# Performance work log

Hardware: AMD Instinct MI355X
Metric: run time of the kernel (lower is better)

## Reference

```python
import jax, jax.numpy as jnp
import numpy as np
import math

EMBED_DIMS = 256
NUM_LANDMARKS = 40  # hard-coded k=40 in the original module
B, N = 2, 8192


def setup_inputs() -> dict:
    key = jax.random.key(0)
    ks = jax.random.split(key, 9)
    C = EMBED_DIMS
    w = lambda k: jax.random.normal(k, (C, C), dtype=jnp.float32) * 0.02
    b = lambda k: jax.random.normal(k, (C,), dtype=jnp.float32) * 0.02
    return {
        "query": jax.random.normal(ks[0], (B, N, C), dtype=jnp.float32),
        "Wq": w(ks[1]), "bq": b(ks[2]),
        "Wk": w(ks[3]), "bk": b(ks[4]),
        "Wv": w(ks[5]), "bv": b(ks[6]),
        "Wo": w(ks[7]), "bo": b(ks[8]),
    }


def reference(query, Wq, bq, Wk, bk, Wv, bv, Wo, bo):
    # key = value = identity = query (defaults in the original forward)
    C = query.shape[-1]
    scaling = math.sqrt(C)

    q = query @ Wq.T + bq  # [B, N, C]
    k = query @ Wk.T + bk
    v = query @ Wv.T + bv

    # Full similarity only to score keys: score_m[b, m] = sum_n sim_nm[b, n, m]
    sim_nm = jnp.einsum('bnc,bmc->bnm', q, k) / scaling  # [B, N, N]
    score_m = sim_nm.sum(axis=1)                          # [B, N]

    _, top_idx = jax.lax.top_k(score_m, NUM_LANDMARKS)    # [B, 40]
    selected = jnp.take_along_axis(k, top_idx[:, :, None], axis=1)  # [B, 40, C]

    sim_qn = jax.nn.softmax(jnp.einsum('bnc,bkc->bnk', q, selected) / scaling, axis=-1)  # [B, N, 40]
    sim_km = jax.nn.softmax(jnp.einsum('bmc,bkc->bmk', k, selected) / scaling, axis=-1)  # [B, N, 40]

    sim_qk = jnp.einsum('bnk,bmk->bnm', sim_qn, sim_km)   # [B, N, N]
    out = jnp.einsum('bnm,bmc->bnc', sim_qk, v)           # [B, N, C]
    out = out @ Wo.T + bo
    return query + out  # identity residual; dropouts are identity at p=0
```

## Files before the change

kernel.cpp:

```cpp
#include <hip/hip_runtime.h>
#include <cstddef>
#include <cstdint>

#define BATCH 2
#define SEQ 8192
#define CH 256
#define NLM 40
#define NLMP 48
#define MROWS (BATCH * SEQ)
#define INV_SCALE 0.0625f
#define NCBLK 256

typedef unsigned short ushort_t;
typedef __attribute__((ext_vector_type(8))) short short8;
typedef __attribute__((ext_vector_type(4))) float floatx4;

__device__ __forceinline__ ushort_t f2bf(float f) {
    unsigned int u = __float_as_uint(f);
    u += 0x7FFFu + ((u >> 16) & 1u);
    return (ushort_t)(u >> 16);
}
__device__ __forceinline__ float bf2f(ushort_t u) {
    return __uint_as_float(((unsigned)u) << 16);
}

__global__ __launch_bounds__(256) void convert_colsum(const float* __restrict__ x,
                                                      ushort_t* __restrict__ xbf,
                                                      float* __restrict__ partial) {
    __shared__ float red[4][256];
    const int b = blockIdx.y;
    const int r0 = blockIdx.x * 32;
    const int t = threadIdx.x;
    const int c4 = (t & 63) * 4;
    const int rg = t >> 6;
    const float* base = x + ((size_t)b * SEQ + r0) * 256;
    ushort_t* obase = xbf + ((size_t)b * SEQ + r0) * 256;
    float4 s = {0.f, 0.f, 0.f, 0.f};
#pragma unroll
    for (int i = 0; i < 8; i++) {
        const int r = rg + i * 4;
        const float4 a = *(const float4*)&base[(size_t)r * 256 + c4];
        uint2 o;
        o.x = f2bf(a.x) | ((unsigned)f2bf(a.y) << 16);
        o.y = f2bf(a.z) | ((unsigned)f2bf(a.w) << 16);
        *(uint2*)&obase[(size_t)r * 256 + c4] = o;
        s.x += a.x; s.y += a.y; s.z += a.z; s.w += a.w;
    }
    *(float4*)&red[rg][c4] = s;
    __syncthreads();
    const float tot = red[0][t] + red[1][t] + red[2][t] + red[3][t];
    partial[((size_t)b * NCBLK + blockIdx.x) * 256 + t] = tot;
}

__global__ __launch_bounds__(1024) void ws_kernel(const float* __restrict__ partial,
                                                  const float* __restrict__ Wq,
                                                  const float* __restrict__ bq,
                                                  const float* __restrict__ Wk,
                                                  float* __restrict__ ws,
                                                  float* __restrict__ tmat) {
    const int b = blockIdx.x;
    __shared__ float xs[256];
    __shared__ float qs[256];
    __shared__ float ppart[4][256];
    const int t = threadIdx.x;
    {
        float* tz = tmat + (size_t)b * NLM * 256;
        for (int i = t; i < NLM * 256; i += 1024) tz[i] = 0.f;
    }
    {
        const int c = t & 255, qd = t >> 8;
        const float* pb = partial + ((size_t)b * NCBLK + qd * 64) * 256 + c;
        float a = 0.f;
#pragma unroll 8
        for (int i = 0; i < 64; i++) a += pb[(size_t)i * 256];
        ppart[qd][c] = a;
    }
    __syncthreads();
    if (t < 256) xs[t] = ppart[0][t] + ppart[1][t] + ppart[2][t] + ppart[3][t];
    __syncthreads();
    const int lane = t & 63, w = t >> 6;
    for (int g = 0; g < 16; g++) {
        const int o = w * 16 + g;
        const float4 wq = *(const float4*)&Wq[(size_t)o * 256 + lane * 4];
        const float4 x4 = *(const float4*)&xs[lane * 4];
        float d = wq.x * x4.x + wq.y * x4.y + wq.z * x4.z + wq.w * x4.w;
#pragma unroll
        for (int off = 32; off >= 1; off >>= 1) d += __shfl_down(d, off);
        if (lane == 0) qs[o] = d + 8192.0f * bq[o];
    }
    __syncthreads();
    const int c = t & 255, part = t >> 8;
    float a = 0.f;
    for (int o = part * 64; o < part * 64 + 64; o++)
        a += Wk[(size_t)o * 256 + c] * qs[o];
    ppart[part][c] = a;
    __syncthreads();
    if (t < 256)
        ws[b * 256 + t] = ppart[0][t] + ppart[1][t] + ppart[2][t] + ppart[3][t];
}

__global__ __launch_bounds__(256) void gemm_qkv_score(const ushort_t* __restrict__ xbf,
                                                      const float* __restrict__ Wq,
                                                      const float* __restrict__ Wk,
                                                      const float* __restrict__ Wv,
                                                      const float* __restrict__ bq,
                                                      const float* __restrict__ bk,
                                                      const float* __restrict__ bv,
                                                      ushort_t* __restrict__ qkv,
                                                      const float* __restrict__ query,
                                                      const float* __restrict__ ws,
                                                      float* __restrict__ score) {
    __shared__ __align__(16) ushort_t As[128 * 72];
    __shared__ __align__(16) ushort_t Bs[64 * 40];
    const int z = blockIdx.z;
    const int t = threadIdx.x;
    const int lane = t & 63;
    const int w = t >> 6;

    if (z == 3) {
        const int blk = blockIdx.y * 4 + blockIdx.x;
#pragma unroll
        for (int i = 0; i < 8; i++) {
            const int g = blk * 32 + i * 4 + w;
            const int b = g >> 13;
            const int m = g & 8191;
            const float4 kv = *(const float4*)&query[(size_t)g * 256 + lane * 4];
            const float4 qs = *(const float4*)&ws[b * 256 + lane * 4];
            float d = kv.x * qs.x + kv.y * qs.y + kv.z * qs.z + kv.w * qs.w;
#pragma unroll
            for (int off = 32; off >= 1; off >>= 1) d += __shfl_down(d, off);
            if (lane == 0) score[(size_t)b * SEQ + m] = d * INV_SCALE;
        }
        return;
    }

    const float* __restrict__ W = (z == 0) ? Wq : (z == 1) ? Wk : Wv;
    const float* __restrict__ bias = (z == 0) ? bq : (z == 1) ? bk : bv;
    ushort_t* __restrict__ out = qkv + (size_t)z * MROWS * 256;
    const int o0 = blockIdx.x * 64;
    const int m0 = blockIdx.y * 128;
    const int quad = lane >> 4;
    const int l16 = lane & 15;

    floatx4 acc[2][4];
#pragma unroll
    for (int rt = 0; rt < 2; rt++)
#pragma unroll
        for (int ct = 0; ct < 4; ct++) acc[rt][ct] = (floatx4){0.f, 0.f, 0.f, 0.f};

    for (int kc = 0; kc < 256; kc += 32) {
#pragma unroll
        for (int u = 0; u < 2; u++) {
            const int cid = t + u * 256;
            const int row = cid >> 2, off = cid & 3;
            *(uint4*)&As[row * 40 + off * 8] =
                *(const uint4*)&xbf[(size_t)(m0 + row) * 256 + kc + off * 8];
        }
        {
            const int row = t >> 2, off = t & 3;
            const float* wp = &W[(size_t)(o0 + row) * 256 + kc + off * 8];
            const float4 a = *(const float4*)wp;
            const float4 c = *(const float4*)(wp + 4);
            uint4 o;
            o.x = f2bf(a.x) | ((unsigned)f2bf(a.y) << 16);
            o.y = f2bf(a.z) | ((unsigned)f2bf(a.w) << 16);
            o.z = f2bf(c.x) | ((unsigned)f2bf(c.y) << 16);
            o.w = f2bf(c.z) | ((unsigned)f2bf(c.w) << 16);
            *(uint4*)&Bs[row * 40 + off * 8] = o;
        }
        __syncthreads();
        short8 a[2], b[4];
#pragma unroll
        for (int rt = 0; rt < 2; rt++)
            a[rt] = *(const short8*)&As[(w * 32 + rt * 16 + l16) * 40 + quad * 8];
#pragma unroll
        for (int ct = 0; ct < 4; ct++)
            b[ct] = *(const short8*)&Bs[(ct * 16 + l16) * 40 + quad * 8];
#pragma unroll
        for (int rt = 0; rt < 2; rt++)
#pragma unroll
            for (int ct = 0; ct < 4; ct++)
                acc[rt][ct] = __builtin_amdgcn_mfma_f32_16x16x32_bf16(
                    a[rt], b[ct], acc[rt][ct], 0, 0, 0);
        __syncthreads();
    }

#pragma unroll
    for (int rt = 0; rt < 2; rt++) {
#pragma unroll
        for (int ct = 0; ct < 4; ct++) {
            const int col = ct * 16 + l16;
            const float bb = bias[o0 + col];
#pragma unroll
            for (int reg = 0; reg < 4; reg++) {
                const int row = w * 32 + rt * 16 + quad * 4 + reg;
                As[row * 72 + col] = f2bf(acc[rt][ct][reg] + bb);
            }
        }
    }
    __syncthreads();
#pragma unroll
    for (int u = 0; u < 4; u++) {
        const int cid = t + u * 256;
        const int row = cid >> 3;
        const int off = (cid & 7) * 8;
        *(uint4*)&out[(size_t)(m0 + row) * 256 + o0 + off] =
            *(const uint4*)&As[row * 72 + off];
    }
}

__global__ __launch_bounds__(1024) void topk_gather(const float* __restrict__ score,
                                                    const ushort_t* __restrict__ kmat,
                                                    ushort_t* __restrict__ sel) {
    const int b = blockIdx.x;
    const int t = threadIdx.x;
    __shared__ unsigned hist[256];
    __shared__ unsigned wsum[64];
    __shared__ unsigned sPrefix, sMask, sRem, sNeq;
    __shared__ int sNgt;
    __shared__ int top[NLM];
    __shared__ unsigned topkey[NLM];

    unsigned key[8];
#pragma unroll
    for (int j = 0; j < 8; j++) {
        const unsigned u = __float_as_uint(score[(size_t)b * SEQ + t + j * 1024]);
        key[j] = u ^ (unsigned)(((int)u >> 31) | 0x80000000);
    }
    if (t == 0) { sPrefix = 0; sMask = 0; sRem = NLM; sNgt = 0; sNeq = 0; }

    for (int lvl = 0; lvl < 4; lvl++) {
        const int shift = 24 - 8 * lvl;
        if (t < 256) hist[t] = 0;
        __syncthreads();
        const unsigned pfx = sPrefix, msk = sMask;
#pragma unroll
        for (int j = 0; j < 8; j++)
            if (((key[j] ^ pfx) & msk) == 0)
                atomicAdd(&hist[(key[j] >> shift) & 255u], 1u);
        __syncthreads();
        if (t < 64) wsum[t] = hist[t * 4] + hist[t * 4 + 1] + hist[t * 4 + 2] + hist[t * 4 + 3];
        __syncthreads();
        if (t == 0) {
            unsigned rem = sRem, cum = 0;
            int g = 63;
            for (; g > 0; g--) { if (cum + wsum[g] >= rem) break; cum += wsum[g]; }
            int d = g * 4 + 3;
            for (; d > g * 4; d--) { if (cum + hist[d] >= rem) break; cum += hist[d]; }
            sRem = rem - cum;
            sPrefix |= ((unsigned)d) << shift;
            sMask |= 255u << shift;
        }
        __syncthreads();
    }
    const unsigned K40 = sPrefix;
    const unsigned rem = sRem;
    const int ngt = NLM - (int)rem;

#pragma unroll
    for (int j = 0; j < 8; j++) {
        if (key[j] > K40) {
            const int slot = atomicAdd(&sNgt, 1);
            top[slot] = t + j * 1024; topkey[slot] = key[j];
        } else if (key[j] == K40) {
            const unsigned e = atomicAdd(&sNeq, 1u);
            if (e < rem) {
                const int slot = ngt + (int)e;
                top[slot] = t + j * 1024; topkey[slot] = key[j];
            }
        }
    }
    __syncthreads();

    if (t < 64) {
        unsigned long long c = (t < NLM)
            ? ((((unsigned long long)(~topkey[t])) << 32) | (unsigned)top[t])
            : 0xFFFFFFFFFFFFFFFFull;
#pragma unroll
        for (int kk = 2; kk <= 64; kk <<= 1) {
#pragma unroll
            for (int j = kk >> 1; j >= 1; j >>= 1) {
                const unsigned long long o = __shfl_xor(c, j);
                const bool takeMin = ((t & kk) == 0) == ((t & j) == 0);
                const bool less = c < o;
                c = (takeMin == less) ? c : o;
            }
        }
        if (t < NLM) top[t] = (int)(c & 0xFFFFFFFFu);
    }
    __syncthreads();

    for (int f = t; f < NLMP * 256; f += 1024) {
        const int j = f >> 8;
        const int cc = f & 255;
        sel[(size_t)b * NLMP * 256 + f] =
            (j < NLM) ? kmat[((size_t)b * SEQ + top[j]) * 256 + cc] : (ushort_t)0;
    }
}

__global__ __launch_bounds__(256, 4) void sim_fused(const ushort_t* __restrict__ qbf,
                                                    const ushort_t* __restrict__ kbf,
                                                    const ushort_t* __restrict__ vbf,
                                                    const ushort_t* __restrict__ sel,
                                                    float* __restrict__ simq,
                                                    float* __restrict__ tmat) {
    __shared__ __align__(16) char smem[43008];
    float (*Ps)[40]  = (float(*)[40])smem;
    ushort_t* Vs     = (ushort_t*)(smem + 10240);
    const int b = blockIdx.y;
    const int n0 = blockIdx.x * 64;
    const int t = threadIdx.x;
    const int lane = t & 63;
    const int w = t >> 6;
    const int quad = lane >> 4;
    const int l16 = lane & 15;
    const ushort_t* __restrict__ A = (blockIdx.z == 0) ? qbf : kbf;
    const ushort_t* __restrict__ Arow = A + ((size_t)b * SEQ + n0 + w * 16 + l16) * 256;
    const ushort_t* __restrict__ Sb = sel + (size_t)b * NLMP * 256 + (size_t)l16 * 256;

    floatx4 acc[3];
#pragma unroll
    for (int ct = 0; ct < 3; ct++) acc[ct] = (floatx4){0.f, 0.f, 0.f, 0.f};

#pragma unroll
    for (int ks = 0; ks < 8; ks++) {
        const int ko = ks * 32 + quad * 8;
        const short8 a  = *(const short8*)&Arow[ko];
        const short8 b0 = *(const short8*)&Sb[ko];
        const short8 b1 = *(const short8*)&Sb[16 * 256 + ko];
        const short8 b2 = *(const short8*)&Sb[32 * 256 + ko];
        acc[0] = __builtin_amdgcn_mfma_f32_16x16x32_bf16(a, b0, acc[0], 0, 0, 0);
        acc[1] = __builtin_amdgcn_mfma_f32_16x16x32_bf16(a, b1, acc[1], 0, 0, 0);
        acc[2] = __builtin_amdgcn_mfma_f32_16x16x32_bf16(a, b2, acc[2], 0, 0, 0);
    }

    const bool v2ok = (l16 < 8);
    float p0[4], p1[4], p2[4];
#pragma unroll
    for (int reg = 0; reg < 4; reg++) {
        const float l0 = acc[0][reg] * INV_SCALE;
        const float l1 = acc[1][reg] * INV_SCALE;
        const float l2 = acc[2][reg] * INV_SCALE;
        float m = fmaxf(l0, l1);
        if (v2ok) m = fmaxf(m, l2);
        m = fmaxf(m, __shfl_xor(m, 1));
        m = fmaxf(m, __shfl_xor(m, 2));
        m = fmaxf(m, __shfl_xor(m, 4));
        m = fmaxf(m, __shfl_xor(m, 8));
        const float e0 = expf(l0 - m);
        const float e1 = expf(l1 - m);
        const float e2 = v2ok ? expf(l2 - m) : 0.f;
        float s = e0 + e1 + e2;
        s += __shfl_xor(s, 1);
        s += __shfl_xor(s, 2);
        s += __shfl_xor(s, 4);
        s += __shfl_xor(s, 8);
        const float inv = 1.f / s;
        p0[reg] = e0 * inv; p1[reg] = e1 * inv; p2[reg] = e2 * inv;
    }

    const int row0 = w * 16 + quad * 4;
    if (blockIdx.z == 0) {
        float* __restrict__ dst = &simq[((size_t)b * SEQ + n0 + row0) * NLM];
#pragma unroll
        for (int reg = 0; reg < 4; reg++) {
            float* __restrict__ d2 = dst + reg * NLM;
            d2[l16] = p0[reg];
            d2[16 + l16] = p1[reg];
            if (v2ok) d2[32 + l16] = p2[reg];
        }
        return;
    }

#pragma unroll
    for (int reg = 0; reg < 4; reg++) {
        Ps[row0 + reg][l16] = p0[reg];
        Ps[row0 + reg][16 + l16] = p1[reg];
        if (v2ok) Ps[row0 + reg][32 + l16] = p2[reg];
    }
#pragma unroll
    for (int u = 0; u < 8; u++) {
        const int cid = t + u * 256;
        const int row = cid >> 5, off = (cid & 31) * 8;
        *(uint4*)&Vs[row * 256 + off] =
            *(const uint4*)&vbf[((size_t)b * SEQ + n0 + row) * 256 + off];
    }
    __syncthreads();

    float tac[40];
#pragma unroll
    for (int j = 0; j < 40; j++) tac[j] = 0.f;

#pragma unroll 2
    for (int m = 0; m < 64; m++) {
        const float vv = bf2f(Vs[m * 256 + t]);
#pragma unroll
        for (int j4 = 0; j4 < 10; j4++) {
            const float4 p = *(const float4*)&Ps[m][j4 * 4];
            tac[j4 * 4 + 0] = fmaf(p.x, vv, tac[j4 * 4 + 0]);
            tac[j4 * 4 + 1] = fmaf(p.y, vv, tac[j4 * 4 + 1]);
            tac[j4 * 4 + 2] = fmaf(p.z, vv, tac[j4 * 4 + 2]);
            tac[j4 * 4 + 3] = fmaf(p.w, vv, tac[j4 * 4 + 3]);
        }
    }
#pragma unroll
    for (int j = 0; j < 40; j++)
        atomicAdd(&tmat[(size_t)b * NLM * 256 + j * 256 + t], tac[j]);
}

__global__ __launch_bounds__(256) void out_pre_kernel(const float* __restrict__ simq,
                                                      const float* __restrict__ tmat,
                                                      ushort_t* __restrict__ outp_bf) {
    __shared__ float Pm[64][40];
    const int g0 = blockIdx.x * 64;
    const int b = g0 >> 13;
    const int t = threadIdx.x;
    float* pflat = &Pm[0][0];
    for (int f = t; f < 64 * NLM; f += 256) pflat[f] = simq[(size_t)g0 * NLM + f];
    float tc[40];
#pragma unroll
    for (int l = 0; l < 40; l++) tc[l] = tmat[(size_t)b * NLM * 256 + l * 256 + t];
    __syncthreads();
#pragma unroll 2
    for (int m = 0; m < 64; m++) {
        float a = 0.f;
#pragma unroll
        for (int j4 = 0; j4 < 10; j4++) {
            const float4 p = *(const float4*)&Pm[m][j4 * 4];
            a = fmaf(p.x, tc[j4 * 4 + 0], a);
            a = fmaf(p.y, tc[j4 * 4 + 1], a);
            a = fmaf(p.z, tc[j4 * 4 + 2], a);
            a = fmaf(p.w, tc[j4 * 4 + 3], a);
        }
        outp_bf[((size_t)g0 + m) * 256 + t] = f2bf(a);
    }
}

__global__ __launch_bounds__(256) void gemm_out(const ushort_t* __restrict__ Abf,
                                                const float* __restrict__ Wo,
                                                const float* __restrict__ bias,
                                                const float* __restrict__ resid,
                                                float* __restrict__ out) {
    __shared__ __align__(16) char smem[128 * 68 * 4];
    ushort_t* As = (ushort_t*)smem;
    ushort_t* Bs = (ushort_t*)(smem + 128 * 40 * 2);
    float* Ft = (float*)smem;
    const int t = threadIdx.x;
    const int o0 = blockIdx.x * 64;
    const int m0 = blockIdx.y * 128;
    const int lane = t & 63;
    const int w = t >> 6;
    const int quad = lane >> 4;
    const int l16 = lane & 15;

    floatx4 acc[2][4];
#pragma unroll
    for (int rt = 0; rt < 2; rt++)
#pragma unroll
        for (int ct = 0; ct < 4; ct++) acc[rt][ct] = (floatx4){0.f, 0.f, 0.f, 0.f};

    for (int kc = 0; kc < 256; kc += 32) {
#pragma unroll
        for (int u = 0; u < 2; u++) {
            const int cid = t + u * 256;
            const int row = cid >> 2, off = cid & 3;
            *(uint4*)&As[row * 40 + off * 8] =
                *(const uint4*)&Abf[(size_t)(m0 + row) * 256 + kc + off * 8];
        }
        {
            const int row = t >> 2, off = t & 3;
            const float* wp = &Wo[(size_t)(o0 + row) * 256 + kc + off * 8];
            const float4 a = *(const float4*)wp;
            const float4 c = *(const float4*)(wp + 4);
            uint4 o;
            o.x = f2bf(a.x) | ((unsigned)f2bf(a.y) << 16);
            o.y = f2bf(a.z) | ((unsigned)f2bf(a.w) << 16);
            o.z = f2bf(c.x) | ((unsigned)f2bf(c.y) << 16);
            o.w = f2bf(c.z) | ((unsigned)f2bf(c.w) << 16);
            *(uint4*)&Bs[row * 40 + off * 8] = o;
        }
        __syncthreads();
        short8 a[2], b[4];
#pragma unroll
        for (int rt = 0; rt < 2; rt++)
            a[rt] = *(const short8*)&As[(w * 32 + rt * 16 + l16) * 40 + quad * 8];
#pragma unroll
        for (int ct = 0; ct < 4; ct++)
            b[ct] = *(const short8*)&Bs[(ct * 16 + l16) * 40 + quad * 8];
#pragma unroll
        for (int rt = 0; rt < 2; rt++)
#pragma unroll
            for (int ct = 0; ct < 4; ct++)
                acc[rt][ct] = __builtin_amdgcn_mfma_f32_16x16x32_bf16(
                    a[rt], b[ct], acc[rt][ct], 0, 0, 0);
        __syncthreads();
    }

#pragma unroll
    for (int rt = 0; rt < 2; rt++) {
#pragma unroll
        for (int ct = 0; ct < 4; ct++) {
            const int col = ct * 16 + l16;
            const float bb = bias[o0 + col];
#pragma unroll
            for (int reg = 0; reg < 4; reg++) {
                const int row = w * 32 + rt * 16 + quad * 4 + reg;
                Ft[row * 68 + col] = acc[rt][ct][reg] + bb;
            }
        }
    }
    __syncthreads();
#pragma unroll
    for (int u = 0; u < 8; u++) {
        const int cid = t + u * 256;
        const int row = cid >> 4;
        const int off = (cid & 15) * 4;
        const float4 v = *(const float4*)&Ft[row * 68 + off];
        const float4 r4 = *(const float4*)&resid[(size_t)(m0 + row) * 256 + o0 + off];
        float4 o;
        o.x = v.x + r4.x; o.y = v.y + r4.y; o.z = v.z + r4.z; o.w = v.w + r4.w;
        *(float4*)&out[(size_t)(m0 + row) * 256 + o0 + off] = o;
    }
}

extern "C" void kernel_launch(void* const* d_in, const int* in_sizes, int n_in,
                              void* d_out, int out_size, void* d_ws, size_t ws_size,
                              hipStream_t stream) {
    const float* query = (const float*)d_in[0];
    const float* Wq = (const float*)d_in[1];
    const float* bq = (const float*)d_in[2];
    const float* Wk = (const float*)d_in[3];
    const float* bk = (const float*)d_in[4];
    const float* Wv = (const float*)d_in[5];
    const float* bv = (const float*)d_in[6];
    const float* Wo = (const float*)d_in[7];
    const float* bo = (const float*)d_in[8];
    float* out = (float*)d_out;

    char* p = (char*)d_ws;
    float* simq  = (float*)p;            p += (size_t)MROWS * NLM * 4;
    ushort_t* selbf = (ushort_t*)p;      p += (size_t)BATCH * NLMP * 256 * 2;
    float* tmat  = (float*)p;            p += (size_t)BATCH * NLM * 256 * 4;
    float* partial = (float*)p;          p += (size_t)BATCH * NCBLK * 256 * 4;
    float* ws    = (float*)p;            p += (size_t)BATCH * 256 * 4;
    float* score = (float*)p;            p += (size_t)BATCH * SEQ * 4;
    ushort_t* qkv = (ushort_t*)p;        p += (size_t)3 * MROWS * 256 * 2;
    ushort_t* xbf = (ushort_t*)p;        p += (size_t)MROWS * 256 * 2;
    ushort_t* qbf = qkv;
    ushort_t* kbf = qkv + (size_t)MROWS * 256;
    ushort_t* vbf = qkv + (size_t)2 * MROWS * 256;
    ushort_t* outp_bf = xbf;

    const dim3 blk(256);

    convert_colsum<<<dim3(SEQ / 32, BATCH), blk, 0, stream>>>(query, xbf, partial);
    ws_kernel<<<dim3(BATCH), dim3(1024), 0, stream>>>(partial, Wq, bq, Wk, ws, tmat);

    gemm_qkv_score<<<dim3(4, MROWS / 128, 4), blk, 0, stream>>>(
        xbf, Wq, Wk, Wv, bq, bk, bv, qkv, query, ws, score);

    topk_gather<<<dim3(BATCH), dim3(1024), 0, stream>>>(score, kbf, selbf);

    sim_fused<<<dim3(SEQ / 64, BATCH, 2), blk, 0, stream>>>(qbf, kbf, vbf, selbf, simq, tmat);

    out_pre_kernel<<<dim3(MROWS / 64), blk, 0, stream>>>(simq, tmat, outp_bf);
    gemm_out<<<dim3(4, MROWS / 128), blk, 0, stream>>>(outp_bf, Wo, bo, query, out);
}
```

Before: 196.7 us.

## Use direct global-to-LDS loads with XOR-swizzled tiles and deeper K step in GEMMs

The QKV and output-projection GEMMs now load the bf16 activation tiles straight into LDS with global_load_lds instead of staging them through registers. The LDS tiles widen to K=64 with an XOR swizzle in place of padding, which halves the number of barrier-separated iterations and aims to avoid bank conflicts. The V tile load in the attention kernel also switches to direct-to-LDS loads. The trade-offs are more LDS per block and a dependence on the swizzle indexing matching the wave-uniform LDS base addressing of the async load.

```diff
diff --git a/kernel.cpp b/kernel.cpp
--- a/kernel.cpp
+++ b/kernel.cpp
@@ -22,6 +22,12 @@
 }
 __device__ __forceinline__ float bf2f(ushort_t u) {
     return __uint_as_float(((unsigned)u) << 16);
+}
+
+__device__ __forceinline__ void gload_lds16(const ushort_t* g, ushort_t* l) {
+    __builtin_amdgcn_global_load_lds(
+        (const __attribute__((address_space(1))) unsigned int*)g,
+        (__attribute__((address_space(3))) unsigned int*)l, 16, 0, 0);
 }
 
 __global__ __launch_bounds__(256) void convert_colsum(const float* __restrict__ x,
@@ -110,8 +116,10 @@
                                                       const float* __restrict__ query,
                                                       const float* __restrict__ ws,
                                                       float* __restrict__ score) {
-    __shared__ __align__(16) ushort_t As[128 * 72];
-    __shared__ __align__(16) ushort_t Bs[64 * 40];
+    __shared__ __align__(16) char smem[24576];
+    ushort_t* As = (ushort_t*)smem;
+    ushort_t* Bs = (ushort_t*)(smem + 16384);
+    ushort_t* Es = (ushort_t*)smem;
     const int z = blockIdx.z;
     const int t = threadIdx.x;
     const int lane = t & 63;
@@ -141,6 +149,7 @@
     const int m0 = blockIdx.y * 128;
     const int quad = lane >> 4;
     const int l16 = lane & 15;
+    const int xsw = l16 & 7;
 
     floatx4 acc[2][4];
 #pragma unroll
@@ -148,17 +157,20 @@
 #pragma unroll
         for (int ct = 0; ct < 4; ct++) acc[rt][ct] = (floatx4){0.f, 0.f, 0.f, 0.f};
 
-    for (int kc = 0; kc < 256; kc += 32) {
+    for (int kc = 0; kc < 256; kc += 64) {
+#pragma unroll
+        for (int q = 0; q < 4; q++) {
+            const int r0 = w * 32 + q * 8;
+            gload_lds16(&xbf[(size_t)(m0 + r0 + (lane >> 3)) * 256 + kc +
+                             (((lane & 7) ^ (lane >> 3)) * 8)],
+                        &As[r0 * 64]);
+        }
 #pragma unroll
         for (int u = 0; u < 2; u++) {
             const int cid = t + u * 256;
-            const int row = cid >> 2, off = cid & 3;
-            *(uint4*)&As[row * 40 + off * 8] =
-                *(const uint4*)&xbf[(size_t)(m0 + row) * 256 + kc + off * 8];
-        }
-        {
-            const int row = t >> 2, off = t & 3;
-            const float* wp = &W[(size_t)(o0 + row) * 256 + kc + off * 8];
+            const int row = cid >> 3;
+            const int cch = cid & 7;
+            const float* wp = &W[(size_t)(o0 + row) * 256 + kc + cch * 8];
             const float4 a = *(const float4*)wp;
             const float4 c = *(const float4*)(wp + 4);
             uint4 o;
@@ -166,22 +178,27 @@
             o.y = f2bf(a.z) | ((unsigned)f2bf(a.w) << 16);
             o.z = f2bf(c.x) | ((unsigned)f2bf(c.y) << 16);
             o.w = f2bf(c.z) | ((unsigned)f2bf(c.w) << 16);
-            *(uint4*)&Bs[row * 40 + off * 8] = o;
-        }
-        __syncthreads();
-        short8 a[2], b[4];
-#pragma unroll
-        for (int rt = 0; rt < 2; rt++)
-            a[rt] = *(const short8*)&As[(w * 32 + rt * 16 + l16) * 40 + quad * 8];
-#pragma unroll
-        for (int ct = 0; ct < 4; ct++)
-            b[ct] = *(const short8*)&Bs[(ct * 16 + l16) * 40 + quad * 8];
-#pragma unroll
-        for (int rt = 0; rt < 2; rt++)
+            *(uint4*)&Bs[row * 64 + ((cch ^ (row & 7)) * 8)] = o;
+        }
+        __syncthreads();
+#pragma unroll
+        for (int s = 0; s < 2; s++) {
+            short8 a[2], bf[4];
+#pragma unroll
+            for (int rt = 0; rt < 2; rt++)
+                a[rt] = *(const short8*)&As[(w * 32 + rt * 16 + l16) * 64 +
+                                            (((s * 4 + quad) ^ xsw) * 8)];
 #pragma unroll
             for (int ct = 0; ct < 4; ct++)
-                acc[rt][ct] = __builtin_amdgcn_mfma_f32_16x16x32_bf16(
-                    a[rt], b[ct], acc[rt][ct], 0, 0, 0);
+                bf[ct] = *(const short8*)&Bs[(ct * 16 + l16) * 64 +
+                                             (((s * 4 + quad) ^ xsw) * 8)];
+#pragma unroll
+            for (int rt = 0; rt < 2; rt++)
+#pragma unroll
+                for (int ct = 0; ct < 4; ct++)
+                    acc[rt][ct] = __builtin_amdgcn_mfma_f32_16x16x32_bf16(
+                        a[rt], bf[ct], acc[rt][ct], 0, 0, 0);
+        }
         __syncthreads();
     }
 
@@ -194,7 +211,7 @@
 #pragma unroll
             for (int reg = 0; reg < 4; reg++) {
                 const int row = w * 32 + rt * 16 + quad * 4 + reg;
-                As[row * 72 + col] = f2bf(acc[rt][ct][reg] + bb);
+                Es[row * 72 + col] = f2bf(acc[rt][ct][reg] + bb);
             }
         }
     }
@@ -205,7 +222,7 @@
         const int row = cid >> 3;
         const int off = (cid & 7) * 8;
         *(uint4*)&out[(size_t)(m0 + row) * 256 + o0 + off] =
-            *(const uint4*)&As[row * 72 + off];
+            *(const uint4*)&Es[row * 72 + off];
     }
 }
 
@@ -380,10 +397,9 @@
     }
 #pragma unroll
     for (int u = 0; u < 8; u++) {
-        const int cid = t + u * 256;
-        const int row = cid >> 5, off = (cid & 31) * 8;
-        *(uint4*)&Vs[row * 256 + off] =
-            *(const uint4*)&vbf[((size_t)b * SEQ + n0 + row) * 256 + off];
+        gload_lds16(&vbf[((size_t)b * SEQ + n0 + w * 2 + u * 8 + (lane >> 5)) * 256 +
+                         (lane & 31) * 8],
+                    &Vs[(w * 2 + u * 8) * 256]);
     }
     __syncthreads();
 
@@ -441,9 +457,9 @@
                                                 const float* __restrict__ bias,
                                                 const float* __restrict__ resid,
                                                 float* __restrict__ out) {
-    __shared__ __align__(16) char smem[128 * 68 * 4];
+    __shared__ __align__(16) char smem[34816];
     ushort_t* As = (ushort_t*)smem;
-    ushort_t* Bs = (ushort_t*)(smem + 128 * 40 * 2);
+    ushort_t* Bs = (ushort_t*)(smem + 16384);
     float* Ft = (float*)smem;
     const int t = threadIdx.x;
     const int o0 = blockIdx.x * 64;
@@ -452,6 +468,7 @@
     const int w = t >> 6;
     const int quad = lane >> 4;
     const int l16 = lane & 15;
+    const int xsw = l16 & 7;
 
     floatx4 acc[2][4];
 #pragma unroll
@@ -459,17 +476,20 @@
 #pragma unroll
         for (int ct = 0; ct < 4; ct++) acc[rt][ct] = (floatx4){0.f, 0.f, 0.f, 0.f};
 
-    for (int kc = 0; kc < 256; kc += 32) {
+    for (int kc = 0; kc < 256; kc += 64) {
+#pragma unroll
+        for (int q = 0; q < 4; q++) {
+            const int r0 = w * 32 + q * 8;
+            gload_lds16(&Abf[(size_t)(m0 + r0 + (lane >> 3)) * 256 + kc +
+                             (((lane & 7) ^ (lane >> 3)) * 8)],
+                        &As[r0 * 64]);
+        }
 #pragma unroll
         for (int u = 0; u < 2; u++) {
             const int cid = t + u * 256;
-            const int row = cid >> 2, off = cid & 3;
-            *(uint4*)&As[row * 40 + off * 8] =
-                *(const uint4*)&Abf[(size_t)(m0 + row) * 256 + kc + off * 8];
-        }
-        {
-            const int row = t >> 2, off = t & 3;
-            const float* wp = &Wo[(size_t)(o0 + row) * 256 + kc + off * 8];
+            const int row = cid >> 3;
+            const int cch = cid & 7;
+            const float* wp = &Wo[(size_t)(o0 + row) * 256 + kc + cch * 8];
             const float4 a = *(const float4*)wp;
             const float4 c = *(const float4*)(wp + 4);
             uint4 o;
@@ -477,22 +497,27 @@
             o.y = f2bf(a.z) | ((unsigned)f2bf(a.w) << 16);
             o.z = f2bf(c.x) | ((unsigned)f2bf(c.y) << 16);
             o.w = f2bf(c.z) | ((unsigned)f2bf(c.w) << 16);
-            *(uint4*)&Bs[row * 40 + off * 8] = o;
-        }
-        __syncthreads();
-        short8 a[2], b[4];
-#pragma unroll
-        for (int rt = 0; rt < 2; rt++)
-            a[rt] = *(const short8*)&As[(w * 32 + rt * 16 + l16) * 40 + quad * 8];
-#pragma unroll
-        for (int ct = 0; ct < 4; ct++)
-            b[ct] = *(const short8*)&Bs[(ct * 16 + l16) * 40 + quad * 8];
-#pragma unroll
-        for (int rt = 0; rt < 2; rt++)
+            *(uint4*)&Bs[row * 64 + ((cch ^ (row & 7)) * 8)] = o;
+        }
+        __syncthreads();
+#pragma unroll
+        for (int s = 0; s < 2; s++) {
+            short8 a[2], bf[4];
+#pragma unroll
+            for (int rt = 0; rt < 2; rt++)
+                a[rt] = *(const short8*)&As[(w * 32 + rt * 16 + l16) * 64 +
+                                            (((s * 4 + quad) ^ xsw) * 8)];
 #pragma unroll
             for (int ct = 0; ct < 4; ct++)
-                acc[rt][ct] = __builtin_amdgcn_mfma_f32_16x16x32_bf16(
-                    a[rt], b[ct], acc[rt][ct], 0, 0, 0);
+                bf[ct] = *(const short8*)&Bs[(ct * 16 + l16) * 64 +
+                                             (((s * 4 + quad) ^ xsw) * 8)];
+#pragma unroll
+            for (int rt = 0; rt < 2; rt++)
+#pragma unroll
+                for (int ct = 0; ct < 4; ct++)
+                    acc[rt][ct] = __builtin_amdgcn_mfma_f32_16x16x32_bf16(
+                        a[rt], bf[ct], acc[rt][ct], 0, 0, 0);
+        }
         __syncthreads();
     }
 
```

After: 191.9 us. 1.03x faster.
